# Kernel optimization log

Measured on AMD Instinct MI355X. Metric: run time of the kernel, lower is better.

Reference implementation:

```python
import jax, jax.numpy as jnp
import numpy as np

VOXEL = 0.8  # meters per grid cell (from `* 0.8` and `/0.8` in source)
GRID = 256   # BEV grid size (from torch.zeros(256, 256))


def _points_in_any_box(points, boxes):
    """points: (M, 3) grid-cell coords shared across batch; boxes: (B, T, 7) as
    (cx, cy, cz, dx, dy, dz, yaw). Returns (B, M) bool: point inside any box.
    Mirrors roiaware_pool3d points_in_boxes_gpu (rotate by -yaw, half-size test)."""
    shift = points[None, :, None, :] - boxes[:, None, :, :3]      # (B, M, T, 3)
    c = jnp.cos(boxes[:, None, :, 6])                              # (B, 1, T)
    s = jnp.sin(boxes[:, None, :, 6])
    rx = shift[..., 0] * c + shift[..., 1] * s                     # local x
    ry = -shift[..., 0] * s + shift[..., 1] * c                    # local y
    half = boxes[:, None, :, 3:6] * 0.5                            # (B, 1, T, 3)
    inb = (jnp.abs(rx) < half[..., 0]) \
        & (jnp.abs(ry) < half[..., 1]) \
        & (jnp.abs(shift[..., 2]) <= half[..., 2])                 # (B, M, T)
    return jnp.any(inb, axis=-1)                                   # (B, M)


def setup_inputs() -> dict:
    key = jax.random.key(0)
    k1, k2, k3, k4, k5, k6 = jax.random.split(key, 6)
    B, C, H, T = 16, 32, GRID, 20
    u1 = jax.random.uniform(k1, (B, C, H, H))
    added = jnp.where(u1 > 0.98, u1, 0.0)
    u2 = jax.random.uniform(k2, (B, C + 1, H, H))
    orig = jnp.where(u2 > 0.98, u2, 0.0)
    # boxes inside the grid extent [0, 256*0.8) meters
    ctr = jax.random.uniform(k3, (B, T, 2), minval=40.0, maxval=160.0)
    cz = jnp.full((B, T, 1), VOXEL)
    dims = jax.random.uniform(k4, (B, T, 3), minval=4.0, maxval=16.0)
    dims = dims.at[..., 2].set(2.0)  # dz covers the fixed point z = 0.8
    yaw = jax.random.uniform(k5, (B, T, 1), minval=-3.14, maxval=3.14)
    boxes = jnp.concatenate([ctr, cz, dims, yaw], axis=-1)
    tf_ego = jax.random.normal(k6, (B, 4, 4))
    return {"added_points": added, "original_points": orig,
            "boxes": boxes, "tf_ego": tf_ego}


def reference(added_points, original_points, boxes, tf_ego):
    B, _, H, W = added_points.shape
    T = boxes.shape[1]
    # collapse channel/height dim -> BEV occupancy maps (B, H, W)
    pred = jnp.sum(added_points, axis=1)
    orig = jnp.sum(original_points[:, 1:], axis=1)
    # every grid cell is a candidate point at (i*0.8, j*0.8, 0.8) (source: nonzero idx * 0.8)
    ii, jj = jnp.meshgrid(jnp.arange(H), jnp.arange(W), indexing='ij')
    pts = jnp.stack([ii.reshape(-1) * VOXEL,
                     jj.reshape(-1) * VOXEL,
                     jnp.full((H * W,), VOXEL)], axis=-1).astype(boxes.dtype)
    in_box = _points_in_any_box(pts, boxes)                        # (B, H*W)
    # keep only occupied cells that fall inside some box -> binary grids
    occ_p = (pred.reshape(B, -1) != 0) & in_box
    occ_o = (orig.reshape(B, -1) != 0) & in_box
    inter = jnp.sum(occ_p & occ_o, axis=-1).astype(jnp.float32)
    union = jnp.sum(occ_p | occ_o, axis=-1).astype(jnp.float32)
    iou_b = inter / jnp.maximum(union, 1.0)                        # per-batch grid IoU
    # source accumulates the (identical) IoU once per box, then divides by batch
    return T * jnp.sum(iou_b) / B
```

## Files before the change

### kernel.cpp

```cpp
#include <hip/hip_runtime.h>
#include <hip/hip_bf16.h>
#include <cstdint>

#define H 256
#define HW (H * H)
#define T_BOX 20
#define WLCAP 3584
#define GBLK 64

__device__ __forceinline__ float bf2f(unsigned short u) {
    union { unsigned int x; float f; } c;
    c.x = ((unsigned int)u) << 16;
    return c.f;
}
__device__ __forceinline__ unsigned short f2bf_bits(float x) {
    union { float f; unsigned int u; } c;
    c.f = x;
    return (unsigned short)((c.u + 0x7fffu + ((c.u >> 16) & 1u)) >> 16);
}
__device__ __forceinline__ float bfq(float x) { return bf2f(f2bf_bits(x)); }

__device__ __forceinline__ bool detect_f32(const void* boxes_) {
    const float* bxf = (const float*)boxes_;
    return (fabsf(bxf[2] - 0.8f) < 0.25f) && (fabsf(bxf[9] - 0.8f) < 0.25f);
}

__global__ __launch_bounds__(256)
void inbox_kernel(const void* __restrict__ boxes_,
                  unsigned int* __restrict__ wl,
                  unsigned int* __restrict__ wl_cnt) {
    __shared__ float s_cx[T_BOX], s_cy[T_BOX], s_sn[T_BOX], s_cs[T_BOX],
                     s_hx[T_BOX], s_hy[T_BOX];

    const int b = blockIdx.x >> 4;
    const int q = blockIdx.x & 15;
    const int t = threadIdx.x;
    const bool is_f32 = detect_f32(boxes_);

    if (t < T_BOX) {
        float cx, cy, cz, dx, dy, dz, yaw, pz;
        if (is_f32) {
            const float* bp = (const float*)boxes_ + ((size_t)b * T_BOX + t) * 7;
            cx = bp[0]; cy = bp[1]; cz = bp[2];
            dx = bp[3]; dy = bp[4]; dz = bp[5]; yaw = bp[6];
            pz = 0.8f;
        } else {
            const unsigned short* bp =
                (const unsigned short*)boxes_ + ((size_t)b * T_BOX + t) * 7;
            cx = bf2f(bp[0]); cy = bf2f(bp[1]); cz = bf2f(bp[2]);
            dx = bf2f(bp[3]); dy = bf2f(bp[4]); dz = bf2f(bp[5]);
            yaw = bf2f(bp[6]);
            pz = bfq(0.8f);
        }
        float hx = 0.5f * dx, hy = 0.5f * dy, hz = 0.5f * dz;
        if (!(fabsf(pz - cz) <= hz)) hx = -1.0f;
        s_cx[t] = cx; s_cy[t] = cy;
        s_sn[t] = sinf(yaw); s_cs[t] = cosf(yaw);
        s_hx[t] = hx; s_hy[t] = hy;
    }
    __syncthreads();

    const int grp = q * 256 + t;
    const int M   = grp * 16;
    const int i   = M >> 8;
    const int j0  = M & 255;
    float px = (float)((double)i * 0.8);
    float py[16];
#pragma unroll
    for (int e = 0; e < 16; ++e) py[e] = (float)((double)(j0 + e) * 0.8);
    if (!is_f32) {
        px = bfq(px);
#pragma unroll
        for (int e = 0; e < 16; ++e) py[e] = bfq(py[e]);
    }

    unsigned int inb = 0;
    for (int k = 0; k < T_BOX; ++k) {
        const float cx = s_cx[k], cy = s_cy[k], sn = s_sn[k], cs = s_cs[k];
        const float hx = s_hx[k], hy = s_hy[k];
        const float sx  = px - cx;
        const float sxc = sx * cs, sxs = sx * sn;
#pragma unroll
        for (int e = 0; e < 16; ++e) {
            const float sy = py[e] - cy;
            const float rx = sxc + sy * sn;
            const float ry = sy * cs - sxs;
            if ((fabsf(rx) < hx) & (fabsf(ry) < hy)) inb |= (1u << e);
        }
    }

    if (inb) {
        const unsigned int pos = atomicAdd(&wl_cnt[b], 1u);
        if (pos < WLCAP) wl[(size_t)b * WLCAP + pos] = ((unsigned int)grp << 16) | inb;
    }
}

__global__ __launch_bounds__(256)
void gather_kernel(const void* __restrict__ added_,
                   const void* __restrict__ orig_,
                   const void* __restrict__ boxes_,
                   const unsigned int* __restrict__ wl,
                   const unsigned int* __restrict__ wl_cnt,
                   unsigned long long* __restrict__ cnt,
                   int Ca, int Co) {
    const bool is_f32 = detect_f32(boxes_);
    const int b    = blockIdx.x / GBLK;
    const int w0   = (blockIdx.x % GBLK) * 4 + (threadIdx.x >> 6);
    const int lane = threadIdx.x & 63;
    const int g    = lane >> 4;
    const int j    = lane & 15;

    const unsigned int n = min(wl_cnt[b], (unsigned int)WLCAP);

    unsigned int inter = 0, uni = 0;

    for (unsigned int e = (unsigned int)w0; e < n; e += GBLK * 4) {
        const unsigned int ent   = wl[(size_t)b * WLCAP + e];
        const unsigned int inb16 = ent & 0xFFFFu;
        const int M = (int)(ent >> 16) * 16 + j;

        unsigned int nzv = 0;
        if (is_f32) {
            const float* base = (g < 2)
                ? (const float*)added_ + ((size_t)b * Ca + g * 16) * HW + M
                : (const float*)orig_  + ((size_t)b * Co + 1 + (g - 2) * 16) * HW + M;
            unsigned int v[16];
#pragma unroll
            for (int i = 0; i < 16; ++i)
                v[i] = *(const unsigned int*)(base + (size_t)i * HW);
#pragma unroll
            for (int i = 0; i < 16; ++i) nzv |= v[i];
        } else {
            const unsigned short* base = (g < 2)
                ? (const unsigned short*)added_ + ((size_t)b * Ca + g * 16) * HW + M
                : (const unsigned short*)orig_  + ((size_t)b * Co + 1 + (g - 2) * 16) * HW + M;
            unsigned short v[16];
#pragma unroll
            for (int i = 0; i < 16; ++i) v[i] = base[(size_t)i * HW];
            unsigned int o = 0;
#pragma unroll
            for (int i = 0; i < 16; ++i) o |= v[i];
            nzv = o;
        }
        const unsigned long long bal = __ballot(nzv != 0u);
        const unsigned int pm = ((unsigned int)bal | (unsigned int)(bal >> 16)) & 0xFFFFu;
        const unsigned int om = ((unsigned int)(bal >> 32) | (unsigned int)(bal >> 48)) & 0xFFFFu;
        inter += __popc(pm & om & inb16);
        uni   += __popc((pm | om) & inb16);
    }

    if (lane == 0 && (inter | uni)) {
        const unsigned long long val =
            ((unsigned long long)inter << 32) | (unsigned long long)uni;
        atomicAdd(&cnt[b], val);
    }
}

__global__ void finish_kernel(const unsigned long long* __restrict__ cnt,
                              unsigned int* __restrict__ out, int B, int T) {
    if (threadIdx.x == 0 && blockIdx.x == 0) {
        float s = 0.0f;
        for (int b = 0; b < B; ++b) {
            unsigned long long v = cnt[b];
            float inter = (float)(unsigned int)(v >> 32);
            float uni   = (float)(unsigned int)(v & 0xffffffffu);
            s += inter / fmaxf(uni, 1.0f);
        }
        const float x = (float)T * s / (float)B;
        const unsigned int h = f2bf_bits(x);
        out[0] = (h << 16) | h;
    }
}

extern "C" void kernel_launch(void* const* d_in, const int* in_sizes, int n_in,
                              void* d_out, int out_size, void* d_ws, size_t ws_size,
                              hipStream_t stream) {
    const void* added = d_in[0];
    const void* orig  = d_in[1];
    const void* boxes = d_in[2];

    const int B  = in_sizes[2] / (T_BOX * 7);
    const int Ca = in_sizes[0] / (B * HW);
    const int Co = in_sizes[1] / (B * HW);

    unsigned long long* cnt = (unsigned long long*)d_ws;
    unsigned int* wl_cnt = (unsigned int*)(cnt + B);
    unsigned int* wl     = wl_cnt + B;
    hipMemsetAsync(d_ws, 0, (size_t)B * 12, stream);

    inbox_kernel<<<B * 16, 256, 0, stream>>>(boxes, wl, wl_cnt);
    gather_kernel<<<B * GBLK, 256, 0, stream>>>(added, orig, boxes,
                                                wl, wl_cnt, cnt, Ca, Co);
    finish_kernel<<<1, 64, 0, stream>>>(cnt, (unsigned int*)d_out, B, T_BOX);
}
```

Measured before the change: 268.3 us.

## Remap gather lanes to load 4 contiguous cells per channel with vector loads

Each lane now handles one channel index and a group of four contiguous grid cells, loading them as one uint4 (or ushort4) per channel slab instead of 16 scalar strided loads. Ballots plus bit-folding reduce the per-lane results to a 16-bit occupancy mask for each of the four channel groups. The aim is fewer, wider memory transactions per worklist entry. In exchange the kernel issues 16 ballots and extra shift/or work per entry, and the alignment of the vector loads depends on 16-cell group offsets.

```diff
diff --git a/kernel.cpp b/kernel.cpp
--- a/kernel.cpp
+++ b/kernel.cpp
@@ -107,44 +107,53 @@
     const int b    = blockIdx.x / GBLK;
     const int w0   = (blockIdx.x % GBLK) * 4 + (threadIdx.x >> 6);
     const int lane = threadIdx.x & 63;
-    const int g    = lane >> 4;
-    const int j    = lane & 15;
+    const int q    = lane >> 4;
+    const int mI   = lane & 15;
 
     const unsigned int n = min(wl_cnt[b], (unsigned int)WLCAP);
+
+    size_t mbase[4];
+    mbase[0] = ((size_t)b * Ca + mI) * HW;
+    mbase[1] = ((size_t)b * Ca + 16 + mI) * HW;
+    mbase[2] = ((size_t)b * Co + 1 + mI) * HW;
+    mbase[3] = ((size_t)b * Co + 17 + mI) * HW;
 
     unsigned int inter = 0, uni = 0;
 
     for (unsigned int e = (unsigned int)w0; e < n; e += GBLK * 4) {
         const unsigned int ent   = wl[(size_t)b * WLCAP + e];
         const unsigned int inb16 = ent & 0xFFFFu;
-        const int M = (int)(ent >> 16) * 16 + j;
-
-        unsigned int nzv = 0;
-        if (is_f32) {
-            const float* base = (g < 2)
-                ? (const float*)added_ + ((size_t)b * Ca + g * 16) * HW + M
-                : (const float*)orig_  + ((size_t)b * Co + 1 + (g - 2) * 16) * HW + M;
-            unsigned int v[16];
-#pragma unroll
-            for (int i = 0; i < 16; ++i)
-                v[i] = *(const unsigned int*)(base + (size_t)i * HW);
-#pragma unroll
-            for (int i = 0; i < 16; ++i) nzv |= v[i];
-        } else {
-            const unsigned short* base = (g < 2)
-                ? (const unsigned short*)added_ + ((size_t)b * Ca + g * 16) * HW + M
-                : (const unsigned short*)orig_  + ((size_t)b * Co + 1 + (g - 2) * 16) * HW + M;
-            unsigned short v[16];
-#pragma unroll
-            for (int i = 0; i < 16; ++i) v[i] = base[(size_t)i * HW];
-            unsigned int o = 0;
-#pragma unroll
-            for (int i = 0; i < 16; ++i) o |= v[i];
-            nzv = o;
-        }
-        const unsigned long long bal = __ballot(nzv != 0u);
-        const unsigned int pm = ((unsigned int)bal | (unsigned int)(bal >> 16)) & 0xFFFFu;
-        const unsigned int om = ((unsigned int)(bal >> 32) | (unsigned int)(bal >> 48)) & 0xFFFFu;
+        const int M0 = (int)(ent >> 16) * 16 + q * 4;
+
+        unsigned int setmask[4];
+#pragma unroll
+        for (int s = 0; s < 4; ++s) {
+            unsigned int c0, c1, c2, c3;
+            if (is_f32) {
+                const uint4 v = *(const uint4*)((const float*)
+                    ((s < 2) ? added_ : orig_) + mbase[s] + M0);
+                c0 = v.x; c1 = v.y; c2 = v.z; c3 = v.w;
+            } else {
+                const ushort4 v = *(const ushort4*)((const unsigned short*)
+                    ((s < 2) ? added_ : orig_) + mbase[s] + M0);
+                c0 = v.x; c1 = v.y; c2 = v.z; c3 = v.w;
+            }
+            unsigned int m16 = 0;
+#pragma unroll
+            for (int p = 0; p < 4; ++p) {
+                const unsigned int cv = (p == 0) ? c0 : (p == 1) ? c1
+                                      : (p == 2) ? c2 : c3;
+                unsigned long long y = __ballot(cv != 0u);
+                y |= y >> 8; y |= y >> 4; y |= y >> 2; y |= y >> 1;
+                m16 |= ((unsigned int)(y & 1ull))         << (0 + p)
+                     | ((unsigned int)((y >> 16) & 1ull)) << (4 + p)
+                     | ((unsigned int)((y >> 32) & 1ull)) << (8 + p)
+                     | ((unsigned int)((y >> 48) & 1ull)) << (12 + p);
+            }
+            setmask[s] = m16;
+        }
+        const unsigned int pm = setmask[0] | setmask[1];
+        const unsigned int om = setmask[2] | setmask[3];
         inter += __popc(pm & om & inb16);
         uni   += __popc((pm | om) & inb16);
     }
```

New measurement: 271.0 us. Within noise of the previous version (+1.0%).
